# Optimization experiments

Hardware: AMD Instinct MI355X
Metric: run time of the kernel (lower is better)

Reference implementation:

```python
import jax, jax.numpy as jnp
import numpy as np

N_NODES = 100000
N_EDGES = 1000000
DIM = 64
N_GRAPHS = 256
OUT_DIM = 10
BN_EPS = 1e-5


def setup_inputs() -> dict:
    key = jax.random.key(0)
    ks = jax.random.split(key, 12)
    s = 0.1  # weight init scale
    x = jax.random.normal(ks[0], (N_NODES, DIM), jnp.float32)
    edge_index = jax.random.randint(ks[1], (2, N_EDGES), 0, N_NODES, dtype=jnp.int32)
    batch = jnp.sort(jax.random.randint(ks[2], (N_NODES,), 0, N_GRAPHS, dtype=jnp.int32))
    w1 = jax.random.normal(ks[3], (3, DIM, DIM), jnp.float32) * s
    b1 = jax.random.normal(ks[4], (3, DIM), jnp.float32) * s
    w2 = jax.random.normal(ks[5], (3, DIM, DIM), jnp.float32) * s
    b2 = jax.random.normal(ks[6], (3, DIM), jnp.float32) * s
    gamma = jax.random.uniform(ks[7], (3, DIM), jnp.float32, 0.5, 1.5)
    beta = jax.random.normal(ks[8], (3, DIM), jnp.float32) * s
    eps_g = jnp.zeros((3,), jnp.float32)  # GIN train_eps, init 0
    lin_w = jax.random.normal(ks[9], (DIM, OUT_DIM), jnp.float32) * s
    lin_b = jax.random.normal(ks[10], (OUT_DIM,), jnp.float32) * s
    return dict(x=x, edge_index=edge_index, batch=batch, w1=w1, b1=b1,
                w2=w2, b2=b2, gamma=gamma, beta=beta, eps_g=eps_g,
                lin_w=lin_w, lin_b=lin_b)


def _gin_layer(x, src, dst, w1, b1, w2, b2, gamma, beta, eps):
    # scatter-add neighbor aggregation: agg[i] = sum_{(j->i) in E} x[j]
    agg = jax.ops.segment_sum(x[src], dst, num_segments=N_NODES)
    h = (1.0 + eps) * x + agg
    h = jax.nn.relu(h @ w1 + b1)
    h = jax.nn.relu(h @ w2 + b2)
    # BatchNorm1d, training-mode batch statistics (biased variance)
    mean = jnp.mean(h, axis=0)
    var = jnp.mean((h - mean) ** 2, axis=0)
    h = (h - mean) * jax.lax.rsqrt(var + BN_EPS) * gamma + beta
    return jax.nn.relu(h)  # outer F.relu(conv(...))


def reference(x, edge_index, batch, w1, b1, w2, b2, gamma, beta, eps_g, lin_w, lin_b):
    src, dst = edge_index[0], edge_index[1]
    for i in range(3):
        x = _gin_layer(x, src, dst, w1[i], b1[i], w2[i], b2[i],
                       gamma[i], beta[i], eps_g[i])
    # global mean pool over graphs
    sums = jax.ops.segment_sum(x, batch, num_segments=N_GRAPHS)
    counts = jax.ops.segment_sum(jnp.ones((x.shape[0],), x.dtype), batch,
                                 num_segments=N_GRAPHS)
    pooled = sums / jnp.maximum(counts, 1.0)[:, None]
    return pooled @ lin_w + lin_b
```

## Files before the change

kernel.cpp:

```cpp
#include <hip/hip_runtime.h>
#include <hip/hip_bf16.h>

#define N_NODES 100000
#define N_EDGES 1000000
#define DIM 64
#define N_GRAPHS 256
#define OUT_DIM 10
#define BN_EPS 1e-5f

#define POOL_BLOCKS 512
#define LAYER_BLOCKS ((N_NODES + 63) / 64)
#define PAD 24
#define SPILL_CAP 8192
#define NPART 8
#define PART_SZ ((N_NODES + NPART - 1) / NPART)

#define XC_BLOCKS ((N_NODES * 16 + 255) / 256)
#define NZERO_WORDS (384 + 16384 + 256 + N_NODES + 16 + 16)
#define NZERO4 (NZERO_WORDS / 4)
#define NZ_BLOCKS ((NZERO4 + 255) / 256)
#define PREP_BLOCKS (6 + XC_BLOCKS + NZ_BLOCKS + 1)

#define FILL_BLOCKS (((N_EDGES + 255) / 256) * NPART)

typedef __bf16 bf16x8 __attribute__((ext_vector_type(8)));
typedef float f32x4 __attribute__((ext_vector_type(4)));

__device__ __forceinline__ float bfu(unsigned short u) {
    return (float)__builtin_bit_cast(__bf16, u);
}

__global__ __launch_bounds__(256) void prep_kernel(
    const float* __restrict__ w1, const float* __restrict__ w2,
    __bf16* __restrict__ wf,
    const float4* __restrict__ x0, ushort4* __restrict__ xp4,
    uint4* __restrict__ zbase,
    unsigned short* __restrict__ xp_s, unsigned short* __restrict__ xq_s,
    unsigned short* __restrict__ xs_s)
{
    const int bid = blockIdx.x;
    const int tid = threadIdx.x;
    if (bid < 6) {
        int L = bid >> 1, mat = bid & 1;
        const float* w = (mat ? w2 : w1) + L * 4096;
        __bf16* dst = wf + bid * 8192;
#pragma unroll
        for (int r = 0; r < 2; ++r) {
            int idx = tid + 256 * r;
            int lane = idx & 63;
            int kt = idx >> 6;
            int kstep = kt >> 2, nt = kt & 3;
            int n = nt * 16 + (lane & 15);
            int kbase = kstep * 32 + (lane >> 4) * 8;
#pragma unroll
            for (int j = 0; j < 8; ++j) {
                float v = w[(kbase + j) * 64 + n];
                __bf16 hi = (__bf16)v;
                dst[idx * 8 + j] = hi;
                dst[4096 + idx * 8 + j] = (__bf16)(v - (float)hi);
            }
        }
    } else if (bid < 6 + XC_BLOCKS) {
        int t = (bid - 6) * 256 + tid;
        if (t < N_NODES * 16) {
            float4 v = x0[t];
            ushort4 o;
            o.x = __builtin_bit_cast(unsigned short, (__bf16)v.x);
            o.y = __builtin_bit_cast(unsigned short, (__bf16)v.y);
            o.z = __builtin_bit_cast(unsigned short, (__bf16)v.z);
            o.w = __builtin_bit_cast(unsigned short, (__bf16)v.w);
            xp4[t] = o;
        }
    } else if (bid < 6 + XC_BLOCKS + NZ_BLOCKS) {
        int i = (bid - 6 - XC_BLOCKS) * 256 + tid;
        if (i < NZERO4) zbase[i] = (uint4){0u, 0u, 0u, 0u};
    } else {
        if (tid < 64) {
            xp_s[tid] = 0;
            xq_s[tid] = 0xFF80;
            xs_s[tid] = 0xFF80;
        }
    }
}

__global__ __launch_bounds__(256) void fill_kernel(
    const int* __restrict__ ei, int* __restrict__ deg,
    int* __restrict__ esrc, int* __restrict__ nspill, int* __restrict__ spill)
{
    const int part = blockIdx.x & (NPART - 1);
    const int e = (blockIdx.x >> 3) * 256 + threadIdx.x;
    if (e >= N_EDGES) return;
    int dst = ei[N_EDGES + e];
    int lo = part * PART_SZ;
    if (dst < lo || dst >= lo + PART_SZ) return;
    int src = ei[e];
    int pos = atomicAdd(&deg[dst], 1);
    if (pos < PAD) {
        esrc[dst * PAD + pos] = src;
    } else {
        int sp = atomicAdd(nspill, 1);
        if (sp < SPILL_CAP) { spill[2 * sp] = dst; spill[2 * sp + 1] = src; }
    }
}

template <bool BN>
__global__ __launch_bounds__(256) void layer_kernel(
    const unsigned short* __restrict__ xb,
    const float* __restrict__ sums_in, const float* __restrict__ gamma,
    const float* __restrict__ beta,
    const int* __restrict__ deg, const int* __restrict__ esrc,
    const int* __restrict__ nspill, const int* __restrict__ spill,
    unsigned short* __restrict__ xbout,
    const __bf16* __restrict__ wf1, const __bf16* __restrict__ wf2,
    const float* __restrict__ b1, const float* __restrict__ b2,
    const float* __restrict__ eps_all, int layer,
    float* __restrict__ sums_out)
{
    __shared__ __attribute__((aligned(16))) unsigned tile[4][16][68];
    __shared__ float bnacc[128];

    const int tid = threadIdx.x;
    const int lane = tid & 63;
    const int wv = tid >> 6;
    const int q = lane >> 4;
    const int r = lane & 15;
    const int node0 = blockIdx.x * 64 + wv * 16;
    const bool active = node0 < N_NODES;

    if (tid < 128) bnacc[tid] = 0.0f;

    float scale = 1.0f, shift = 0.0f;
    if (BN) {
        const float inv_n = 1.0f / (float)N_NODES;
        float mean = sums_in[lane] * inv_n;
        float var = sums_in[64 + lane] * inv_n - mean * mean;
        scale = gamma[lane] * rsqrtf(var + BN_EPS);
        shift = fmaf(-mean, scale, beta[lane]);
    }

    f32x4 acc[4];
    float bs[4], bq[4];
#pragma unroll
    for (int nt = 0; nt < 4; ++nt) {
        acc[nt] = (f32x4){0.f, 0.f, 0.f, 0.f};
        bs[nt] = 0.0f; bq[nt] = 0.0f;
    }

    if (active) {
        const float epsv = 1.0f + eps_all[layer];

        int dvec = 0;
        if (lane < 16) dvec = deg[node0 + lane];
        uint4 nf0, nf1, nf2;
        {
            const uint4* ip = (const uint4*)(esrc + (size_t)node0 * PAD);
            nf0 = ip[0]; nf1 = ip[1]; nf2 = ip[2];
        }
        for (int i = 0; i < 16; ++i) {
            const uint4 c0 = nf0, c1 = nf1, c2 = nf2;
            if (i < 15) {
                const uint4* ip = (const uint4*)(esrc + (size_t)(node0 + i + 1) * PAD);
                nf0 = ip[0]; nf1 = ip[1]; nf2 = ip[2];
            }
            const int n = node0 + i;
            const int dfull = __builtin_amdgcn_readlane(dvec, i);
            const int d = min(dfull, PAD);

            float xv = bfu(xb[(size_t)n * 64 + lane]);
            if (BN) xv = fmaxf(fmaf(xv, scale, shift), 0.0f);
            float hval = epsv * xv;

            {
                unsigned idx[12] = {c0.x, c0.y, c0.z, c0.w, c1.x, c1.y,
                                    c1.z, c1.w, c2.x, c2.y, c2.z, c2.w};
                unsigned short u[12];
#pragma unroll
                for (int j = 0; j < 12; ++j) {
                    unsigned s = idx[j];
                    s = (s < (unsigned)N_NODES) ? s : (unsigned)N_NODES;
                    u[j] = xb[(size_t)s * 64 + lane];
                }
#pragma unroll
                for (int j = 0; j < 12; ++j) {
                    float t = bfu(u[j]);
                    if (BN) t = fmaxf(fmaf(t, scale, shift), 0.0f);
                    hval += t;
                }
            }
            if (d > 12) {
                const int* ep = esrc + (size_t)n * PAD + 12;
                unsigned short u[12];
#pragma unroll
                for (int j = 0; j < 12; ++j) {
                    unsigned s = (unsigned)ep[j];
                    s = (s < (unsigned)N_NODES) ? s : (unsigned)N_NODES;
                    u[j] = xb[(size_t)s * 64 + lane];
                }
#pragma unroll
                for (int j = 0; j < 12; ++j) {
                    float t = bfu(u[j]);
                    if (BN) t = fmaxf(fmaf(t, scale, shift), 0.0f);
                    hval += t;
                }
            }
            if (dfull > PAD) {
                int ns = min(*nspill, SPILL_CAP);
                for (int e = 0; e < ns; ++e) {
                    if (spill[2 * e] == n) {
                        float t = bfu(xb[(size_t)spill[2 * e + 1] * 64 + lane]);
                        if (BN) t = fmaxf(fmaf(t, scale, shift), 0.0f);
                        hval += t;
                    }
                }
            }
            __bf16 hi = (__bf16)hval;
            __bf16 lo = (__bf16)(hval - (float)hi);
            tile[wv][i][lane] = ((unsigned)__builtin_bit_cast(unsigned short, hi) << 16)
                              | (unsigned)__builtin_bit_cast(unsigned short, lo);
        }

        uint4 f0 = *(const uint4*)&tile[wv][r][q * 8];
        uint4 f1 = *(const uint4*)&tile[wv][r][q * 8 + 4];
        uint4 f2 = *(const uint4*)&tile[wv][r][32 + q * 8];
        uint4 f3 = *(const uint4*)&tile[wv][r][32 + q * 8 + 4];
#pragma unroll
        for (int kstep = 0; kstep < 2; ++kstep) {
            uint4 p0 = kstep ? f2 : f0;
            uint4 p1 = kstep ? f3 : f1;
            unsigned pk[8] = {p0.x, p0.y, p0.z, p0.w, p1.x, p1.y, p1.z, p1.w};
            bf16x8 ahi, alo;
#pragma unroll
            for (int j = 0; j < 8; ++j) {
                ahi[j] = __builtin_bit_cast(__bf16, (unsigned short)(pk[j] >> 16));
                alo[j] = __builtin_bit_cast(__bf16, (unsigned short)(pk[j] & 0xffffu));
            }
#pragma unroll
            for (int nt = 0; nt < 4; ++nt) {
                const __bf16* bp = wf1 + ((kstep * 4 + nt) * 64 + lane) * 8;
                bf16x8 bhi = *(const bf16x8*)bp;
                bf16x8 blo = *(const bf16x8*)(bp + 4096);
                acc[nt] = __builtin_amdgcn_mfma_f32_16x16x32_bf16(ahi, bhi, acc[nt], 0, 0, 0);
                acc[nt] = __builtin_amdgcn_mfma_f32_16x16x32_bf16(alo, bhi, acc[nt], 0, 0, 0);
                acc[nt] = __builtin_amdgcn_mfma_f32_16x16x32_bf16(ahi, blo, acc[nt], 0, 0, 0);
            }
        }
#pragma unroll
        for (int nt = 0; nt < 4; ++nt) {
            float b1v = b1[nt * 16 + r];
#pragma unroll
            for (int reg = 0; reg < 4; ++reg) {
                float v = fmaxf(acc[nt][reg] + b1v, 0.0f);
                __bf16 hi = (__bf16)v;
                __bf16 lo = (__bf16)(v - (float)hi);
                unsigned pk = ((unsigned)__builtin_bit_cast(unsigned short, hi) << 16)
                            | (unsigned)__builtin_bit_cast(unsigned short, lo);
                tile[wv][q * 4 + reg][nt * 16 + r] = pk;
            }
            acc[nt] = (f32x4){0.f, 0.f, 0.f, 0.f};
        }
#pragma unroll
        for (int kstep = 0; kstep < 2; ++kstep) {
            uint4 p0 = *(const uint4*)&tile[wv][r][kstep * 32 + q * 8];
            uint4 p1 = *(const uint4*)&tile[wv][r][kstep * 32 + q * 8 + 4];
            unsigned pk[8] = {p0.x, p0.y, p0.z, p0.w, p1.x, p1.y, p1.z, p1.w};
            bf16x8 ahi, alo;
#pragma unroll
            for (int j = 0; j < 8; ++j) {
                ahi[j] = __builtin_bit_cast(__bf16, (unsigned short)(pk[j] >> 16));
                alo[j] = __builtin_bit_cast(__bf16, (unsigned short)(pk[j] & 0xffffu));
            }
#pragma unroll
            for (int nt = 0; nt < 4; ++nt) {
                const __bf16* bp = wf2 + ((kstep * 4 + nt) * 64 + lane) * 8;
                bf16x8 bhi = *(const bf16x8*)bp;
                bf16x8 blo = *(const bf16x8*)(bp + 4096);
                acc[nt] = __builtin_amdgcn_mfma_f32_16x16x32_bf16(ahi, bhi, acc[nt], 0, 0, 0);
                acc[nt] = __builtin_amdgcn_mfma_f32_16x16x32_bf16(alo, bhi, acc[nt], 0, 0, 0);
                acc[nt] = __builtin_amdgcn_mfma_f32_16x16x32_bf16(ahi, blo, acc[nt], 0, 0, 0);
            }
        }
#pragma unroll
        for (int nt = 0; nt < 4; ++nt) {
            float b2v = b2[nt * 16 + r];
#pragma unroll
            for (int reg = 0; reg < 4; ++reg) {
                float v = fmaxf(acc[nt][reg] + b2v, 0.0f);
                size_t oi = (size_t)(node0 + q * 4 + reg) * 64 + nt * 16 + r;
                xbout[oi] = __builtin_bit_cast(unsigned short, (__bf16)v);
                bs[nt] += v;
                bq[nt] = fmaf(v, v, bq[nt]);
            }
        }
    }
    __syncthreads();
#pragma unroll
    for (int nt = 0; nt < 4; ++nt) {
        float s = bs[nt];
        s += __shfl_xor(s, 16);
        s += __shfl_xor(s, 32);
        float ss = bq[nt];
        ss += __shfl_xor(ss, 16);
        ss += __shfl_xor(ss, 32);
        if (q == 0) {
            atomicAdd(&bnacc[nt * 16 + r], s);
            atomicAdd(&bnacc[64 + nt * 16 + r], ss);
        }
    }
    __syncthreads();
    if (tid < 128) unsafeAtomicAdd(&sums_out[tid], bnacc[tid]);
}

__global__ __launch_bounds__(256) void pool_kernel(
    const unsigned short* __restrict__ h2b, const float* __restrict__ sums,
    const float* __restrict__ gamma, const float* __restrict__ beta,
    const int* __restrict__ batch,
    float* __restrict__ pooled, float* __restrict__ counts)
{
    const int lane = threadIdx.x & 63;
    const int w = blockIdx.x * 4 + (threadIdx.x >> 6);
    const int nw = POOL_BLOCKS * 4;
    const int npw = (N_NODES + nw - 1) / nw;
    int n0 = w * npw;
    if (n0 >= N_NODES) return;
    int n1 = min(n0 + npw, N_NODES);

    const float inv_n = 1.0f / (float)N_NODES;
    float mean = sums[lane] * inv_n;
    float var = sums[64 + lane] * inv_n - mean * mean;
    const float scale = gamma[lane] * rsqrtf(var + BN_EPS);
    const float shift = fmaf(-mean, scale, beta[lane]);

    int cur = batch[n0];
    float acc = 0.0f, cnt = 0.0f;
    for (int n = n0; n < n1; ++n) {
        int g = batch[n];
        if (g != cur) {
            unsafeAtomicAdd(&pooled[cur * 64 + lane], acc);
            if (lane == 0) unsafeAtomicAdd(&counts[cur], cnt);
            acc = 0.0f; cnt = 0.0f; cur = g;
        }
        float v = bfu(h2b[(size_t)n * 64 + lane]);
        v = fmaxf(fmaf(v, scale, shift), 0.0f);
        acc += v;
        cnt += 1.0f;
    }
    unsafeAtomicAdd(&pooled[cur * 64 + lane], acc);
    if (lane == 0) unsafeAtomicAdd(&counts[cur], cnt);
}

__global__ __launch_bounds__(256) void final_kernel(
    const float* __restrict__ pooled, const float* __restrict__ counts,
    const float* __restrict__ lin_w, const float* __restrict__ lin_b,
    float* __restrict__ out)
{
    int t = blockIdx.x * 256 + threadIdx.x;
    if (t >= N_GRAPHS * OUT_DIM) return;
    int g = t / OUT_DIM;
    int o = t - g * OUT_DIM;
    float acc = 0.0f;
#pragma unroll 8
    for (int d = 0; d < 64; ++d)
        acc = fmaf(pooled[g * 64 + d], lin_w[d * OUT_DIM + o], acc);
    float c = fmaxf(counts[g], 1.0f);
    out[t] = acc / c + lin_b[o];
}

extern "C" void kernel_launch(void* const* d_in, const int* in_sizes, int n_in,
                              void* d_out, int out_size, void* d_ws, size_t ws_size,
                              hipStream_t stream)
{
    const float* x0    = (const float*)d_in[0];
    const int*   ei    = (const int*)d_in[1];
    const int*   batch = (const int*)d_in[2];
    const float* w1    = (const float*)d_in[3];
    const float* b1    = (const float*)d_in[4];
    const float* w2    = (const float*)d_in[5];
    const float* b2    = (const float*)d_in[6];
    const float* gamma = (const float*)d_in[7];
    const float* beta  = (const float*)d_in[8];
    const float* eps_g = (const float*)d_in[9];
    const float* lin_w = (const float*)d_in[10];
    const float* lin_b = (const float*)d_in[11];
    float* out = (float*)d_out;

    float* ws   = (float*)d_ws;
    float* SUMS = ws;
    float* POOL = SUMS + 384;
    float* CNT  = POOL + N_GRAPHS * 64;
    int*   DEG    = (int*)(CNT + N_GRAPHS);
    int*   NSPILL = DEG + N_NODES;
    int*   PFCNT  = NSPILL + 16;
    __bf16* WF  = (__bf16*)(PFCNT + 16);
    int*   SPILL  = (int*)(WF + 6 * 8192);
    int*   ESRC   = SPILL + 2 * SPILL_CAP;
    unsigned short* XP = (unsigned short*)(ESRC + (size_t)N_NODES * PAD);
    unsigned short* XQ = XP + (size_t)(N_NODES + 1) * 64;
    unsigned short* XS = XQ + (size_t)(N_NODES + 1) * 64;
    unsigned short* XR = XS + (size_t)(N_NODES + 1) * 64;

    prep_kernel<<<PREP_BLOCKS, 256, 0, stream>>>(
        w1, w2, WF, (const float4*)x0, (ushort4*)XP, (uint4*)SUMS,
        XP + (size_t)N_NODES * 64, XQ + (size_t)N_NODES * 64,
        XS + (size_t)N_NODES * 64);
    fill_kernel<<<FILL_BLOCKS, 256, 0, stream>>>(ei, DEG, ESRC, NSPILL, SPILL);

    layer_kernel<false><<<LAYER_BLOCKS, 256, 0, stream>>>(
        XP, nullptr, nullptr, nullptr, DEG, ESRC, NSPILL, SPILL, XQ,
        WF, WF + 8192, b1, b2, eps_g, 0, SUMS);

    layer_kernel<true><<<LAYER_BLOCKS, 256, 0, stream>>>(
        XQ, SUMS, gamma, beta, DEG, ESRC, NSPILL, SPILL, XS,
        WF + 16384, WF + 24576, b1 + 64, b2 + 64, eps_g, 1, SUMS + 128);

    layer_kernel<true><<<LAYER_BLOCKS, 256, 0, stream>>>(
        XS, SUMS + 128, gamma + 64, beta + 64, DEG, ESRC, NSPILL, SPILL, XR,
        WF + 32768, WF + 40960, b1 + 128, b2 + 128, eps_g, 2, SUMS + 256);

    pool_kernel<<<POOL_BLOCKS, 256, 0, stream>>>(
        XR, SUMS + 256, gamma + 128, beta + 128, batch, POOL, CNT);
    final_kernel<<<(N_GRAPHS * OUT_DIM + 255) / 256, 256, 0, stream>>>(
        POOL, CNT, lin_w, lin_b, out);
}
```

Before: 353.7 us.

## Bucket edges by partition once, then place; fuse pooling and linear head

Edge binning no longer re-reads the whole edge list once per destination partition. A build pass compacts (dst,src) pairs into per-partition buckets using wave ballots and a block-level atomic reservation, and a place pass then scatters each bucket into the padded adjacency. The pool and final kernels are replaced by one head kernel with one block per graph, using graph start offsets computed from the sorted batch array. This removes atomics and a launch at the cost of an extra intermediate bucket buffer, which reuses the XR region, and a fixed bucket capacity.

```diff
diff --git a/kernel.cpp b/kernel.cpp
--- a/kernel.cpp
+++ b/kernel.cpp
@@ -8,20 +8,24 @@
 #define OUT_DIM 10
 #define BN_EPS 1e-5f
 
-#define POOL_BLOCKS 512
 #define LAYER_BLOCKS ((N_NODES + 63) / 64)
 #define PAD 24
 #define SPILL_CAP 8192
 #define NPART 8
 #define PART_SZ ((N_NODES + NPART - 1) / NPART)
 
+#define EDGE_BLOCKS ((N_EDGES + 255) / 256)
 #define XC_BLOCKS ((N_NODES * 16 + 255) / 256)
-#define NZERO_WORDS (384 + 16384 + 256 + N_NODES + 16 + 16)
-#define NZERO4 (NZERO_WORDS / 4)
-#define NZ_BLOCKS ((NZERO4 + 255) / 256)
-#define PREP_BLOCKS (6 + XC_BLOCKS + NZ_BLOCKS + 1)
-
-#define FILL_BLOCKS (((N_EDGES + 255) / 256) * NPART)
+#define BUILD_BLOCKS (EDGE_BLOCKS + XC_BLOCKS + 6 + 1)
+
+#define BUCK_CAP 131072
+#define PLACE_BLOCKS ((BUCK_CAP / 256) * NPART)
+
+#define Z4A 96
+#define Z4B 25008
+#define ZLIN_BLOCKS ((Z4A + Z4B + 255) / 256)
+#define SEG_BLOCKS ((N_NODES + 255) / 256)
+#define ZERO_BLOCKS (ZLIN_BLOCKS + SEG_BLOCKS)
 
 typedef __bf16 bf16x8 __attribute__((ext_vector_type(8)));
 typedef float f32x4 __attribute__((ext_vector_type(4)));
@@ -30,38 +34,75 @@
     return (float)__builtin_bit_cast(__bf16, u);
 }
 
-__global__ __launch_bounds__(256) void prep_kernel(
+__global__ __launch_bounds__(256) void zero_kernel(
+    uint4* __restrict__ za, uint4* __restrict__ zb,
+    const int* __restrict__ batch, int* __restrict__ bstart)
+{
+    const int bid = blockIdx.x;
+    const int tid = threadIdx.x;
+    if (bid < ZLIN_BLOCKS) {
+        int i = bid * 256 + tid;
+        uint4 z = {0u, 0u, 0u, 0u};
+        if (i < Z4A) za[i] = z;
+        else if (i < Z4A + Z4B) zb[i - Z4A] = z;
+    } else {
+        int n = (bid - ZLIN_BLOCKS) * 256 + tid;
+        if (n < N_NODES) {
+            int b = batch[n];
+            int bp = (n == 0) ? -1 : batch[n - 1];
+            for (int gg = bp + 1; gg <= b; ++gg) bstart[gg] = n;
+            if (n == N_NODES - 1)
+                for (int gg = b + 1; gg <= N_GRAPHS; ++gg) bstart[gg] = N_NODES;
+        }
+    }
+}
+
+__global__ __launch_bounds__(256) void build_kernel(
+    const int* __restrict__ ei, int* __restrict__ pfcnt,
+    int2* __restrict__ buck,
     const float* __restrict__ w1, const float* __restrict__ w2,
     __bf16* __restrict__ wf,
     const float4* __restrict__ x0, ushort4* __restrict__ xp4,
-    uint4* __restrict__ zbase,
     unsigned short* __restrict__ xp_s, unsigned short* __restrict__ xq_s,
     unsigned short* __restrict__ xs_s)
 {
+    __shared__ int lcnt[NPART];
+    __shared__ int gbase[NPART];
     const int bid = blockIdx.x;
     const int tid = threadIdx.x;
-    if (bid < 6) {
-        int L = bid >> 1, mat = bid & 1;
-        const float* w = (mat ? w2 : w1) + L * 4096;
-        __bf16* dst = wf + bid * 8192;
-#pragma unroll
-        for (int r = 0; r < 2; ++r) {
-            int idx = tid + 256 * r;
-            int lane = idx & 63;
-            int kt = idx >> 6;
-            int kstep = kt >> 2, nt = kt & 3;
-            int n = nt * 16 + (lane & 15);
-            int kbase = kstep * 32 + (lane >> 4) * 8;
-#pragma unroll
-            for (int j = 0; j < 8; ++j) {
-                float v = w[(kbase + j) * 64 + n];
-                __bf16 hi = (__bf16)v;
-                dst[idx * 8 + j] = hi;
-                dst[4096 + idx * 8 + j] = (__bf16)(v - (float)hi);
-            }
-        }
-    } else if (bid < 6 + XC_BLOCKS) {
-        int t = (bid - 6) * 256 + tid;
+
+    if (bid < EDGE_BLOCKS) {
+        const int e = bid * 256 + tid;
+        int dstv = -1, srcv = 0;
+        if (e < N_EDGES) { dstv = ei[N_EDGES + e]; srcv = ei[e]; }
+        int p = (dstv >= 0) ? (dstv / PART_SZ) : -1;
+
+        if (tid < NPART) lcnt[tid] = 0;
+        __syncthreads();
+        int lbase = 0, rank = 0;
+        for (int pp = 0; pp < NPART; ++pp) {
+            unsigned long long mask = __ballot(p == pp);
+            if (mask == 0ull) continue;
+            int leader = __ffsll(mask) - 1;
+            int m = __popcll(mask);
+            int wb = 0;
+            if ((tid & 63) == leader) wb = atomicAdd(&lcnt[pp], m);
+            wb = __shfl(wb, leader, 64);
+            if (p == pp) {
+                lbase = wb;
+                rank = __popcll(mask & ((1ull << (unsigned)(tid & 63)) - 1ull));
+            }
+        }
+        __syncthreads();
+        if (tid < NPART) gbase[tid] = atomicAdd(&pfcnt[tid], lcnt[tid]);
+        __syncthreads();
+        if (p >= 0) {
+            int slot = gbase[p] + lbase + rank;
+            if (slot < BUCK_CAP)
+                buck[(size_t)p * BUCK_CAP + slot] = (int2){dstv, srcv};
+        }
+    } else if (bid < EDGE_BLOCKS + XC_BLOCKS) {
+        int t = (bid - EDGE_BLOCKS) * 256 + tid;
         if (t < N_NODES * 16) {
             float4 v = x0[t];
             ushort4 o;
@@ -71,9 +112,27 @@
             o.w = __builtin_bit_cast(unsigned short, (__bf16)v.w);
             xp4[t] = o;
         }
-    } else if (bid < 6 + XC_BLOCKS + NZ_BLOCKS) {
-        int i = (bid - 6 - XC_BLOCKS) * 256 + tid;
-        if (i < NZERO4) zbase[i] = (uint4){0u, 0u, 0u, 0u};
+    } else if (bid < EDGE_BLOCKS + XC_BLOCKS + 6) {
+        int wb = bid - EDGE_BLOCKS - XC_BLOCKS;
+        int L = wb >> 1, mat = wb & 1;
+        const float* w = (mat ? w2 : w1) + L * 4096;
+        __bf16* dst = wf + wb * 8192;
+#pragma unroll
+        for (int r = 0; r < 2; ++r) {
+            int idx = tid + 256 * r;
+            int lane = idx & 63;
+            int kt = idx >> 6;
+            int kstep = kt >> 2, nt = kt & 3;
+            int n = nt * 16 + (lane & 15);
+            int kbase = kstep * 32 + (lane >> 4) * 8;
+#pragma unroll
+            for (int j = 0; j < 8; ++j) {
+                float v = w[(kbase + j) * 64 + n];
+                __bf16 hi = (__bf16)v;
+                dst[idx * 8 + j] = hi;
+                dst[4096 + idx * 8 + j] = (__bf16)(v - (float)hi);
+            }
+        }
     } else {
         if (tid < 64) {
             xp_s[tid] = 0;
@@ -83,23 +142,23 @@
     }
 }
 
-__global__ __launch_bounds__(256) void fill_kernel(
-    const int* __restrict__ ei, int* __restrict__ deg,
-    int* __restrict__ esrc, int* __restrict__ nspill, int* __restrict__ spill)
-{
-    const int part = blockIdx.x & (NPART - 1);
-    const int e = (blockIdx.x >> 3) * 256 + threadIdx.x;
-    if (e >= N_EDGES) return;
-    int dst = ei[N_EDGES + e];
-    int lo = part * PART_SZ;
-    if (dst < lo || dst >= lo + PART_SZ) return;
-    int src = ei[e];
-    int pos = atomicAdd(&deg[dst], 1);
+__global__ __launch_bounds__(256) void place_kernel(
+    const int* __restrict__ pfcnt, const int2* __restrict__ buck,
+    int* __restrict__ deg, int* __restrict__ esrc,
+    int* __restrict__ nspill, int* __restrict__ spill)
+{
+    const int p = blockIdx.x & (NPART - 1);
+    const int i = (blockIdx.x >> 3) * 256 + threadIdx.x;
+    int n = pfcnt[p];
+    n = n < BUCK_CAP ? n : BUCK_CAP;
+    if (i >= n) return;
+    int2 pr = buck[(size_t)p * BUCK_CAP + i];
+    int pos = atomicAdd(&deg[pr.x], 1);
     if (pos < PAD) {
-        esrc[dst * PAD + pos] = src;
+        esrc[pr.x * PAD + pos] = pr.y;
     } else {
         int sp = atomicAdd(nspill, 1);
-        if (sp < SPILL_CAP) { spill[2 * sp] = dst; spill[2 * sp + 1] = src; }
+        if (sp < SPILL_CAP) { spill[2 * sp] = pr.x; spill[2 * sp + 1] = pr.y; }
     }
 }
 
@@ -310,19 +369,20 @@
     if (tid < 128) unsafeAtomicAdd(&sums_out[tid], bnacc[tid]);
 }
 
-__global__ __launch_bounds__(256) void pool_kernel(
+__global__ __launch_bounds__(1024) void head_kernel(
     const unsigned short* __restrict__ h2b, const float* __restrict__ sums,
     const float* __restrict__ gamma, const float* __restrict__ beta,
-    const int* __restrict__ batch,
-    float* __restrict__ pooled, float* __restrict__ counts)
-{
-    const int lane = threadIdx.x & 63;
-    const int w = blockIdx.x * 4 + (threadIdx.x >> 6);
-    const int nw = POOL_BLOCKS * 4;
-    const int npw = (N_NODES + nw - 1) / nw;
-    int n0 = w * npw;
-    if (n0 >= N_NODES) return;
-    int n1 = min(n0 + npw, N_NODES);
+    const int* __restrict__ bstart, const float* __restrict__ lin_w,
+    const float* __restrict__ lin_b, float* __restrict__ out)
+{
+    __shared__ float red[16][64];
+    __shared__ float pooled_s[64];
+    const int g = blockIdx.x;
+    const int tid = threadIdx.x;
+    const int lane = tid & 63;
+    const int wv = tid >> 6;
+    const int lo = bstart[g];
+    const int hi = bstart[g + 1];
 
     const float inv_n = 1.0f / (float)N_NODES;
     float mean = sums[lane] * inv_n;
@@ -330,39 +390,28 @@
     const float scale = gamma[lane] * rsqrtf(var + BN_EPS);
     const float shift = fmaf(-mean, scale, beta[lane]);
 
-    int cur = batch[n0];
-    float acc = 0.0f, cnt = 0.0f;
-    for (int n = n0; n < n1; ++n) {
-        int g = batch[n];
-        if (g != cur) {
-            unsafeAtomicAdd(&pooled[cur * 64 + lane], acc);
-            if (lane == 0) unsafeAtomicAdd(&counts[cur], cnt);
-            acc = 0.0f; cnt = 0.0f; cur = g;
-        }
+    float acc = 0.0f;
+    for (int n = lo + wv; n < hi; n += 16) {
         float v = bfu(h2b[(size_t)n * 64 + lane]);
-        v = fmaxf(fmaf(v, scale, shift), 0.0f);
-        acc += v;
-        cnt += 1.0f;
-    }
-    unsafeAtomicAdd(&pooled[cur * 64 + lane], acc);
-    if (lane == 0) unsafeAtomicAdd(&counts[cur], cnt);
-}
-
-__global__ __launch_bounds__(256) void final_kernel(
-    const float* __restrict__ pooled, const float* __restrict__ counts,
-    const float* __restrict__ lin_w, const float* __restrict__ lin_b,
-    float* __restrict__ out)
-{
-    int t = blockIdx.x * 256 + threadIdx.x;
-    if (t >= N_GRAPHS * OUT_DIM) return;
-    int g = t / OUT_DIM;
-    int o = t - g * OUT_DIM;
-    float acc = 0.0f;
-#pragma unroll 8
-    for (int d = 0; d < 64; ++d)
-        acc = fmaf(pooled[g * 64 + d], lin_w[d * OUT_DIM + o], acc);
-    float c = fmaxf(counts[g], 1.0f);
-    out[t] = acc / c + lin_b[o];
+        acc += fmaxf(fmaf(v, scale, shift), 0.0f);
+    }
+    red[wv][lane] = acc;
+    __syncthreads();
+    if (wv == 0) {
+        float s = 0.0f;
+#pragma unroll
+        for (int w = 0; w < 16; ++w) s += red[w][lane];
+        float c = fmaxf((float)(hi - lo), 1.0f);
+        pooled_s[lane] = s / c;
+    }
+    __syncthreads();
+    if (tid < OUT_DIM) {
+        float a2 = lin_b[tid];
+#pragma unroll
+        for (int d = 0; d < 64; ++d)
+            a2 = fmaf(pooled_s[d], lin_w[d * OUT_DIM + tid], a2);
+        out[g * OUT_DIM + tid] = a2;
+    }
 }
 
 extern "C" void kernel_launch(void* const* d_in, const int* in_sizes, int n_in,
@@ -398,11 +447,19 @@
     unsigned short* XS = XQ + (size_t)(N_NODES + 1) * 64;
     unsigned short* XR = XS + (size_t)(N_NODES + 1) * 64;
 
-    prep_kernel<<<PREP_BLOCKS, 256, 0, stream>>>(
-        w1, w2, WF, (const float4*)x0, (ushort4*)XP, (uint4*)SUMS,
+    int*  BSTART = (int*)POOL;
+    int2* BUCK   = (int2*)XR;
+
+    zero_kernel<<<ZERO_BLOCKS, 256, 0, stream>>>(
+        (uint4*)SUMS, (uint4*)DEG, batch, BSTART);
+
+    build_kernel<<<BUILD_BLOCKS, 256, 0, stream>>>(
+        ei, PFCNT, BUCK, w1, w2, WF, (const float4*)x0, (ushort4*)XP,
         XP + (size_t)N_NODES * 64, XQ + (size_t)N_NODES * 64,
         XS + (size_t)N_NODES * 64);
-    fill_kernel<<<FILL_BLOCKS, 256, 0, stream>>>(ei, DEG, ESRC, NSPILL, SPILL);
+
+    place_kernel<<<PLACE_BLOCKS, 256, 0, stream>>>(
+        PFCNT, BUCK, DEG, ESRC, NSPILL, SPILL);
 
     layer_kernel<false><<<LAYER_BLOCKS, 256, 0, stream>>>(
         XP, nullptr, nullptr, nullptr, DEG, ESRC, NSPILL, SPILL, XQ,
@@ -416,8 +473,6 @@
         XS, SUMS + 128, gamma + 64, beta + 64, DEG, ESRC, NSPILL, SPILL, XR,
         WF + 32768, WF + 40960, b1 + 128, b2 + 128, eps_g, 2, SUMS + 256);
 
-    pool_kernel<<<POOL_BLOCKS, 256, 0, stream>>>(
-        XR, SUMS + 256, gamma + 128, beta + 128, batch, POOL, CNT);
-    final_kernel<<<(N_GRAPHS * OUT_DIM + 255) / 256, 256, 0, stream>>>(
-        POOL, CNT, lin_w, lin_b, out);
-}
+    head_kernel<<<N_GRAPHS, 1024, 0, stream>>>(
+        XR, SUMS + 256, gamma + 128, beta + 128, BSTART, lin_w, lin_b, out);
+}
```

After: 381.4 us. +7.8%, slower.
